# Kernel tuning notes

Hardware: AMD Instinct MI355X
Metric: run time of the kernel (lower is better)

Reference implementation:

```python
import jax, jax.numpy as jnp
import numpy as np

N = 50000      # nodes
E = 800000     # edges
D = 128        # feature dim
L = 3          # gcn layers
EPS = 1e-5     # batchnorm eps


def setup_inputs() -> dict:
    key = jax.random.key(0)
    ks = jax.random.split(key, 6)
    s = (2.0 / (D + D)) ** 0.5  # xavier-uniform scale proxy
    x = jax.random.normal(ks[0], (N, D), jnp.float32)
    edge_index = jax.random.randint(ks[1], (2, E), 0, N, dtype=jnp.int32)
    conv_w = jax.random.normal(ks[2], (L, D, D), jnp.float32) * s
    conv_b = jnp.zeros((L, D), jnp.float32)
    bn_gamma = jnp.ones((2, D), jnp.float32)
    bn_beta = jnp.zeros((2, D), jnp.float32)
    mlp_w = jax.random.normal(ks[3], (2, D, D), jnp.float32) * s
    mlp_b = jnp.zeros((2, D), jnp.float32)
    out_w = jax.random.normal(ks[4], (D, 1), jnp.float32) * s
    out_b = jnp.zeros((1,), jnp.float32)
    return dict(x=x, edge_index=edge_index, conv_w=conv_w, conv_b=conv_b,
                bn_gamma=bn_gamma, bn_beta=bn_beta, mlp_w=mlp_w, mlp_b=mlp_b,
                out_w=out_w, out_b=out_b)


def _batchnorm(h, gamma, beta):
    # train-mode BN: batch stats over nodes (biased variance, as torch uses for normalization)
    mean = jnp.mean(h, axis=0)
    var = jnp.mean((h - mean) ** 2, axis=0)
    return (h - mean) * jax.lax.rsqrt(var + EPS) * gamma + beta


def reference(x, conv_w, conv_b, bn_gamma, bn_beta, mlp_w, mlp_b, out_w, out_b, edge_index):
    # --- GCN normalization (PyG GCNConv default: add self-loops, sym norm) ---
    loops = jnp.arange(N, dtype=edge_index.dtype)
    src = jnp.concatenate([edge_index[0], loops])  # [E+N]
    dst = jnp.concatenate([edge_index[1], loops])
    deg = jax.ops.segment_sum(jnp.ones_like(dst, jnp.float32), dst, num_segments=N)
    dis = jnp.where(deg > 0, jax.lax.rsqrt(jnp.maximum(deg, 1.0)), 0.0)  # deg^-1/2
    norm = (dis[src] * dis[dst])[:, None]  # [E+N, 1]

    def gcn_conv(h, W, b):
        h = h @ W                                     # [N, D] transform
        msg = h[src] * norm                           # gather + scale, [E+N, D]
        return jax.ops.segment_sum(msg, dst, num_segments=N) + b

    # dropout is identity (training=False)
    h = x
    # layers 0..L-2: conv -> bn -> relu
    for layer in range(L - 1):
        h = gcn_conv(h, conv_w[layer], conv_b[layer])
        h = _batchnorm(h, bn_gamma[layer], bn_beta[layer])
        h = jax.nn.relu(h)
    # last conv: relu(conv), then bns[-1] applied AGAIN (faithful to original quirk)
    h = jax.nn.relu(gcn_conv(h, conv_w[L - 1], conv_b[L - 1]))
    h = _batchnorm(h, bn_gamma[-1], bn_beta[-1])

    # --- MLP classifier head: relu hidden layers, sigmoid output ---
    for i in range(mlp_w.shape[0]):
        h = jax.nn.relu(h @ mlp_w[i] + mlp_b[i])
    out = jax.nn.sigmoid(h @ out_w + out_b)  # [N, 1]
    return out
```

## Files before the change

kernel.cpp:

```cpp
#include <hip/hip_runtime.h>
#include <hip/hip_bf16.h>

#define NN 50000
#define EE 800000
#define DD 128

typedef __attribute__((ext_vector_type(8))) short short8;
typedef __attribute__((ext_vector_type(4))) float floatx4;

__device__ __forceinline__ unsigned short f2bf(float f) {
    unsigned int x = __float_as_uint(f);
    unsigned int r = x + 0x7fffu + ((x >> 16) & 1u);
    return (unsigned short)(r >> 16);
}
__device__ __forceinline__ float2 bf2x2(unsigned int u) {
    return make_float2(__uint_as_float(u << 16), __uint_as_float(u & 0xffff0000u));
}

__global__ void k_deg(const int* __restrict__ ei, int* __restrict__ deg) {
    int e = blockIdx.x * 256 + threadIdx.x;
    if (e < EE) {
        int d = ei[EE + e];
        if (d >= 0 && d < NN) atomicAdd(&deg[d], 1);
    }
}

__global__ void k_scan_block(const int* __restrict__ deg, int* __restrict__ scanned,
                             int* __restrict__ blocksum) {
    __shared__ int lds[256];
    int t = threadIdx.x;
    int i = blockIdx.x * 256 + t;
    int v = (i < NN) ? deg[i] : 0;
    lds[t] = v;
    __syncthreads();
    for (int off = 1; off < 256; off <<= 1) {
        int add = (t >= off) ? lds[t - off] : 0;
        __syncthreads();
        lds[t] += add;
        __syncthreads();
    }
    if (i < NN) scanned[i] = lds[t];
    if (t == 255) blocksum[blockIdx.x] = lds[255];
}

__global__ void k_scan_final(const int* __restrict__ deg, const int* __restrict__ scanned,
                             const int* __restrict__ blocksum, int nb,
                             int* __restrict__ rowptr, int* __restrict__ cursor,
                             float* __restrict__ dis) {
    __shared__ int lds[256];
    int t = threadIdx.x;
    int v = (t < nb) ? blocksum[t] : 0;
    lds[t] = v;
    __syncthreads();
    for (int off = 1; off < 256; off <<= 1) {
        int add = (t >= off) ? lds[t - off] : 0;
        __syncthreads();
        lds[t] += add;
        __syncthreads();
    }
    int boff = (blockIdx.x == 0) ? 0 : lds[blockIdx.x - 1];
    if (blockIdx.x == 0 && t == 0) rowptr[NN] = lds[nb - 1];
    int i = blockIdx.x * 256 + t;
    if (i < NN) {
        int rv = scanned[i] - deg[i] + boff;
        rowptr[i] = rv;
        cursor[i] = rv;
        dis[i] = rsqrtf((float)deg[i] + 1.0f);
    }
}

__global__ void k_fill(const int* __restrict__ ei, int* __restrict__ cursor,
                       int* __restrict__ csr) {
    int e = blockIdx.x * 256 + threadIdx.x;
    if (e < EE) {
        int s = ei[e];
        int d = ei[EE + e];
        if ((unsigned)s < (unsigned)NN && (unsigned)d < (unsigned)NN) {
            int pos = atomicAdd(&cursor[d], 1);
            csr[pos] = s;
        }
    }
}

__global__ void k_ell(const int* __restrict__ rowptr, const int* __restrict__ csr,
                      int* __restrict__ ell) {
    int t = blockIdx.x * 256 + threadIdx.x;
    if (t >= NN * 32) return;
    int r = t >> 5, slot = t & 31;
    int beg = rowptr[r];
    int d = rowptr[r + 1] - beg;
    ell[t] = (slot < d) ? csr[beg + slot] : NN;
}

__global__ void k_wprep(const float* __restrict__ conv_w, const float* __restrict__ mlp_w,
                        unsigned short* __restrict__ Wf, unsigned int* __restrict__ hsrow) {
    int g = blockIdx.x * 256 + threadIdx.x;
    if (g < 81920) {
        int m = g >> 14;
        int idx = g & 16383;
        int j  = idx & 7;
        int n  = (idx >> 3) & 15;
        int q  = (idx >> 7) & 3;
        int kk = (idx >> 9) & 3;
        int nt = (idx >> 11) & 1;
        int w  = (idx >> 12) & 3;
        int k = kk * 32 + q * 8 + j;
        int c = w * 32 + nt * 16 + n;
        const float* src = (m < 3) ? (conv_w + m * 16384) : (mlp_w + (m - 3) * 16384);
        Wf[g] = f2bf(src[k * 128 + c]);
    } else if (g - 81920 < 64) {
        hsrow[g - 81920] = 0u;
    }
}

#define LSTR 136
template<int PRO>
__global__ __launch_bounds__(256) void k_gemm_conv(const float* __restrict__ IN,
                                                   const unsigned short* __restrict__ Wf,
                                                   const float* __restrict__ dis,
                                                   const float* __restrict__ cs,
                                                   const float* __restrict__ css,
                                                   const float* __restrict__ gamma,
                                                   const float* __restrict__ beta,
                                                   unsigned short* __restrict__ OUT) {
    __shared__ unsigned short Al[64 * LSTR];
    __shared__ float bnscL[128], bnshL[128];
    const int tid = threadIdx.x;
    const int lane = tid & 63;
    const int w = tid >> 6;
    const int row0 = blockIdx.x * 64;

    if (PRO) {
        if (tid < 128) {
            const float invn = 1.f / (float)NN;
            float mean = cs[tid] * invn;
            float var = css[tid] * invn - mean * mean;
            float sc = gamma[tid] * rsqrtf(fmaxf(var, 0.f) + 1e-5f);
            bnscL[tid] = sc;
            bnshL[tid] = beta[tid] - mean * sc;
        }
        __syncthreads();
    }

    short8 bf[2][4];
    {
        const uint4* Wq = (const uint4*)Wf;
#pragma unroll
        for (int nt = 0; nt < 2; ++nt)
#pragma unroll
            for (int kk = 0; kk < 4; ++kk) {
                uint4 u = Wq[((w * 2 + nt) * 4 + kk) * 64 + lane];
                bf[nt][kk] = *(short8*)&u;
            }
    }

    {
        int r = tid >> 2, kq = (tid & 3) * 32;
        int gr = row0 + r;
        unsigned short tmp[32];
#pragma unroll
        for (int i = 0; i < 8; ++i) {
            float4 v = make_float4(0.f, 0.f, 0.f, 0.f);
            if (gr < NN) v = *(const float4*)&IN[(size_t)gr * DD + kq + i * 4];
            if (PRO) {
                float4 sc = *(const float4*)&bnscL[kq + i * 4];
                float4 sh = *(const float4*)&bnshL[kq + i * 4];
                v.x = fmaf(v.x, sc.x, sh.x);
                v.y = fmaf(v.y, sc.y, sh.y);
                v.z = fmaf(v.z, sc.z, sh.z);
                v.w = fmaf(v.w, sc.w, sh.w);
                v.x = fmaxf(v.x, 0.f); v.y = fmaxf(v.y, 0.f);
                v.z = fmaxf(v.z, 0.f); v.w = fmaxf(v.w, 0.f);
            }
            tmp[i * 4 + 0] = f2bf(v.x); tmp[i * 4 + 1] = f2bf(v.y);
            tmp[i * 4 + 2] = f2bf(v.z); tmp[i * 4 + 3] = f2bf(v.w);
        }
#pragma unroll
        for (int j = 0; j < 4; ++j)
            *(uint4*)&Al[r * LSTR + kq + j * 8] = ((uint4*)tmp)[j];
    }
    __syncthreads();

    const int n = lane & 15, q = lane >> 4;
    floatx4 acc[4][2];
#pragma unroll
    for (int mt = 0; mt < 4; ++mt)
#pragma unroll
        for (int nt = 0; nt < 2; ++nt)
            acc[mt][nt] = (floatx4){0.f, 0.f, 0.f, 0.f};

#pragma unroll
    for (int kk = 0; kk < 4; ++kk) {
        int ko = kk * 32 + q * 8;
#pragma unroll
        for (int mt = 0; mt < 4; ++mt) {
            short8 a = *(const short8*)&Al[(mt * 16 + n) * LSTR + ko];
            acc[mt][0] = __builtin_amdgcn_mfma_f32_16x16x32_bf16(a, bf[0][kk], acc[mt][0], 0, 0, 0);
            acc[mt][1] = __builtin_amdgcn_mfma_f32_16x16x32_bf16(a, bf[1][kk], acc[mt][1], 0, 0, 0);
        }
    }

#pragma unroll
    for (int mt = 0; mt < 4; ++mt) {
#pragma unroll
        for (int reg = 0; reg < 4; ++reg) {
            int r = row0 + mt * 16 + q * 4 + reg;
            if (r < NN) {
                float sc = dis[r];
                OUT[(size_t)r * DD + w * 32 + n]      = f2bf(acc[mt][0][reg] * sc);
                OUT[(size_t)r * DD + w * 32 + 16 + n] = f2bf(acc[mt][1][reg] * sc);
            }
        }
    }
}

__global__ __launch_bounds__(256) void k_mlp_head(const float* __restrict__ IN,
                                                  const unsigned short* __restrict__ Wf4,
                                                  const unsigned short* __restrict__ Wf5,
                                                  const float* __restrict__ b4,
                                                  const float* __restrict__ b5,
                                                  const float* __restrict__ cs,
                                                  const float* __restrict__ css,
                                                  const float* __restrict__ gamma,
                                                  const float* __restrict__ beta,
                                                  const float* __restrict__ ow,
                                                  const float* __restrict__ ob,
                                                  float* __restrict__ out) {
    __shared__ unsigned short Al[64 * LSTR];
    __shared__ float bnscL[128], bnshL[128];
    __shared__ float redH[4][64];
    const int tid = threadIdx.x;
    const int lane = tid & 63;
    const int w = tid >> 6;
    const int row0 = blockIdx.x * 64;
    const int n = lane & 15, q = lane >> 4;

    if (tid < 128) {
        const float invn = 1.f / (float)NN;
        float mean = cs[tid] * invn;
        float var = css[tid] * invn - mean * mean;
        float sc = gamma[tid] * rsqrtf(fmaxf(var, 0.f) + 1e-5f);
        bnscL[tid] = sc;
        bnshL[tid] = beta[tid] - mean * sc;
    }
    __syncthreads();

    {
        int r = tid >> 2, kq = (tid & 3) * 32;
        int gr = row0 + r;
        unsigned short tmp[32];
#pragma unroll
        for (int i = 0; i < 8; ++i) {
            float4 v = make_float4(0.f, 0.f, 0.f, 0.f);
            if (gr < NN) v = *(const float4*)&IN[(size_t)gr * DD + kq + i * 4];
            float4 sc = *(const float4*)&bnscL[kq + i * 4];
            float4 sh = *(const float4*)&bnshL[kq + i * 4];
            v.x = fmaf(v.x, sc.x, sh.x);
            v.y = fmaf(v.y, sc.y, sh.y);
            v.z = fmaf(v.z, sc.z, sh.z);
            v.w = fmaf(v.w, sc.w, sh.w);
            tmp[i * 4 + 0] = f2bf(v.x); tmp[i * 4 + 1] = f2bf(v.y);
            tmp[i * 4 + 2] = f2bf(v.z); tmp[i * 4 + 3] = f2bf(v.w);
        }
#pragma unroll
        for (int j = 0; j < 4; ++j)
            *(uint4*)&Al[r * LSTR + kq + j * 8] = ((uint4*)tmp)[j];
    }
    __syncthreads();

    floatx4 acc[4][2];
#pragma unroll
    for (int mt = 0; mt < 4; ++mt)
#pragma unroll
        for (int nt = 0; nt < 2; ++nt)
            acc[mt][nt] = (floatx4){0.f, 0.f, 0.f, 0.f};
    {
        const uint4* Wq = (const uint4*)Wf4;
#pragma unroll
        for (int kk = 0; kk < 4; ++kk) {
            uint4 u0 = Wq[((w * 2 + 0) * 4 + kk) * 64 + lane];
            uint4 u1 = Wq[((w * 2 + 1) * 4 + kk) * 64 + lane];
            int ko = kk * 32 + q * 8;
#pragma unroll
            for (int mt = 0; mt < 4; ++mt) {
                short8 a = *(const short8*)&Al[(mt * 16 + n) * LSTR + ko];
                acc[mt][0] = __builtin_amdgcn_mfma_f32_16x16x32_bf16(a, *(short8*)&u0, acc[mt][0], 0, 0, 0);
                acc[mt][1] = __builtin_amdgcn_mfma_f32_16x16x32_bf16(a, *(short8*)&u1, acc[mt][1], 0, 0, 0);
            }
        }
    }
    __syncthreads();

    {
        float b0c = b4[w * 32 + n], b1c = b4[w * 32 + 16 + n];
#pragma unroll
        for (int mt = 0; mt < 4; ++mt) {
#pragma unroll
            for (int reg = 0; reg < 4; ++reg) {
                int r = mt * 16 + q * 4 + reg;
                Al[r * LSTR + w * 32 + n]      = f2bf(fmaxf(acc[mt][0][reg] + b0c, 0.f));
                Al[r * LSTR + w * 32 + 16 + n] = f2bf(fmaxf(acc[mt][1][reg] + b1c, 0.f));
            }
        }
    }
    __syncthreads();

#pragma unroll
    for (int mt = 0; mt < 4; ++mt)
#pragma unroll
        for (int nt = 0; nt < 2; ++nt)
            acc[mt][nt] = (floatx4){0.f, 0.f, 0.f, 0.f};
    {
        const uint4* Wq = (const uint4*)Wf5;
#pragma unroll
        for (int kk = 0; kk < 4; ++kk) {
            uint4 u0 = Wq[((w * 2 + 0) * 4 + kk) * 64 + lane];
            uint4 u1 = Wq[((w * 2 + 1) * 4 + kk) * 64 + lane];
            int ko = kk * 32 + q * 8;
#pragma unroll
            for (int mt = 0; mt < 4; ++mt) {
                short8 a = *(const short8*)&Al[(mt * 16 + n) * LSTR + ko];
                acc[mt][0] = __builtin_amdgcn_mfma_f32_16x16x32_bf16(a, *(short8*)&u0, acc[mt][0], 0, 0, 0);
                acc[mt][1] = __builtin_amdgcn_mfma_f32_16x16x32_bf16(a, *(short8*)&u1, acc[mt][1], 0, 0, 0);
            }
        }
    }
    {
        float b0c = b5[w * 32 + n], b1c = b5[w * 32 + 16 + n];
        float w0c = ow[w * 32 + n], w1c = ow[w * 32 + 16 + n];
#pragma unroll
        for (int mt = 0; mt < 4; ++mt) {
#pragma unroll
            for (int reg = 0; reg < 4; ++reg) {
                float h0 = fmaxf(acc[mt][0][reg] + b0c, 0.f);
                float h1 = fmaxf(acc[mt][1][reg] + b1c, 0.f);
                float p = fmaf(h0, w0c, h1 * w1c);
                p += __shfl_xor(p, 1);
                p += __shfl_xor(p, 2);
                p += __shfl_xor(p, 4);
                p += __shfl_xor(p, 8);
                if (n == 0) redH[w][mt * 16 + q * 4 + reg] = p;
            }
        }
        __syncthreads();
        if (tid < 64) {
            int r = row0 + tid;
            if (r < NN) {
                float z = (redH[0][tid] + redH[1][tid]) + (redH[2][tid] + redH[3][tid]) + ob[0];
                out[r] = 1.f / (1.f + expf(-z));
            }
        }
    }
}
#undef LSTR

template<int RELU>
__global__ __launch_bounds__(256) void k_gather(const int* __restrict__ rowptr,
                                                const int* __restrict__ csr,
                                                const int* __restrict__ ell,
                                                const uint4* __restrict__ HSq,
                                                const float* __restrict__ dis,
                                                const float* __restrict__ bias,
                                                float* __restrict__ OUT,
                                                float* __restrict__ colsum,
                                                float* __restrict__ colsumsq) {
    const int tid = threadIdx.x;
    const int lane = tid & 63;
    const int wid = tid >> 6;
    const int c = lane & 15;
    const int jj = lane >> 4;
    const int gwave = blockIdx.x * 4 + wid;

    float4 bia0 = ((const float4*)bias)[2 * c];
    float4 bia1 = ((const float4*)bias)[2 * c + 1];
    float sum[8], sq[8];
#pragma unroll
    for (int t = 0; t < 8; ++t) { sum[t] = 0.f; sq[t] = 0.f; }

    for (int r = gwave; r < NN; r += 8192) {
        int beg = rowptr[r], end = rowptr[r + 1];
        int d = end - beg;
        float a[8];
#pragma unroll
        for (int t = 0; t < 8; ++t) a[t] = 0.f;

        if (jj == 0) {
            uint4 u = HSq[(size_t)r * 16 + c];
            float2 p0 = bf2x2(u.x), p1 = bf2x2(u.y), p2 = bf2x2(u.z), p3 = bf2x2(u.w);
            a[0] += p0.x; a[1] += p0.y; a[2] += p1.x; a[3] += p1.y;
            a[4] += p2.x; a[5] += p2.y; a[6] += p3.x; a[7] += p3.y;
        }

        if (d <= 32) {
            const int4* e4 = (const int4*)(ell + r * 32);
            int4 ia = e4[jj];
            int4 ib = e4[jj + 4];
            uint4 v0 = HSq[(size_t)ia.x * 16 + c];
            uint4 v1 = HSq[(size_t)ia.y * 16 + c];
            uint4 v2 = HSq[(size_t)ia.z * 16 + c];
            uint4 v3 = HSq[(size_t)ia.w * 16 + c];
            uint4 v4 = HSq[(size_t)ib.x * 16 + c];
            uint4 v5 = HSq[(size_t)ib.y * 16 + c];
            uint4 v6 = HSq[(size_t)ib.z * 16 + c];
            uint4 v7 = HSq[(size_t)ib.w * 16 + c];
            uint4 vs[8] = {v0, v1, v2, v3, v4, v5, v6, v7};
#pragma unroll
            for (int t = 0; t < 8; ++t) {
                float2 p0 = bf2x2(vs[t].x), p1 = bf2x2(vs[t].y);
                float2 p2 = bf2x2(vs[t].z), p3 = bf2x2(vs[t].w);
                a[0] += p0.x; a[1] += p0.y; a[2] += p1.x; a[3] += p1.y;
                a[4] += p2.x; a[5] += p2.y; a[6] += p3.x; a[7] += p3.y;
            }
        } else {
            int e1 = end - 1;
            for (int j = beg; j < end; j += 16) {
                int i0 = j + jj, i1 = j + 4 + jj, i2 = j + 8 + jj, i3 = j + 12 + jj;
                int s0 = csr[min(i0, e1)];
                int s1 = csr[min(i1, e1)];
                int s2 = csr[min(i2, e1)];
                int s3 = csr[min(i3, e1)];
                uint4 v0 = HSq[(size_t)s0 * 16 + c];
                uint4 v1 = HSq[(size_t)s1 * 16 + c];
                uint4 v2 = HSq[(size_t)s2 * 16 + c];
                uint4 v3 = HSq[(size_t)s3 * 16 + c];
                if (i0 < end) {
                    float2 p0 = bf2x2(v0.x), p1 = bf2x2(v0.y), p2 = bf2x2(v0.z), p3 = bf2x2(v0.w);
                    a[0] += p0.x; a[1] += p0.y; a[2] += p1.x; a[3] += p1.y;
                    a[4] += p2.x; a[5] += p2.y; a[6] += p3.x; a[7] += p3.y;
                }
                if (i1 < end) {
                    float2 p0 = bf2x2(v1.x), p1 = bf2x2(v1.y), p2 = bf2x2(v1.z), p3 = bf2x2(v1.w);
                    a[0] += p0.x; a[1] += p0.y; a[2] += p1.x; a[3] += p1.y;
                    a[4] += p2.x; a[5] += p2.y; a[6] += p3.x; a[7] += p3.y;
                }
                if (i2 < end) {
                    float2 p0 = bf2x2(v2.x), p1 = bf2x2(v2.y), p2 = bf2x2(v2.z), p3 = bf2x2(v2.w);
                    a[0] += p0.x; a[1] += p0.y; a[2] += p1.x; a[3] += p1.y;
                    a[4] += p2.x; a[5] += p2.y; a[6] += p3.x; a[7] += p3.y;
                }
                if (i3 < end) {
                    float2 p0 = bf2x2(v3.x), p1 = bf2x2(v3.y), p2 = bf2x2(v3.z), p3 = bf2x2(v3.w);
                    a[0] += p0.x; a[1] += p0.y; a[2] += p1.x; a[3] += p1.y;
                    a[4] += p2.x; a[5] += p2.y; a[6] += p3.x; a[7] += p3.y;
                }
            }
        }

#pragma unroll
        for (int t = 0; t < 8; ++t) {
            a[t] += __shfl_xor(a[t], 16);
            a[t] += __shfl_xor(a[t], 32);
        }

        if (jj == 0) {
            float dr = dis[r];
            float v[8];
            v[0] = fmaf(dr, a[0], bia0.x); v[1] = fmaf(dr, a[1], bia0.y);
            v[2] = fmaf(dr, a[2], bia0.z); v[3] = fmaf(dr, a[3], bia0.w);
            v[4] = fmaf(dr, a[4], bia1.x); v[5] = fmaf(dr, a[5], bia1.y);
            v[6] = fmaf(dr, a[6], bia1.z); v[7] = fmaf(dr, a[7], bia1.w);
            if (RELU) {
#pragma unroll
                for (int t = 0; t < 8; ++t) v[t] = fmaxf(v[t], 0.f);
            }
            float* op = OUT + (size_t)r * DD + c * 8;
            *(float4*)op       = make_float4(v[0], v[1], v[2], v[3]);
            *(float4*)(op + 4) = make_float4(v[4], v[5], v[6], v[7]);
#pragma unroll
            for (int t = 0; t < 8; ++t) { sum[t] += v[t]; sq[t] += v[t] * v[t]; }
        }
    }

    __shared__ float redS[4][16][8];
    __shared__ float redQ[4][16][8];
    if (jj == 0) {
#pragma unroll
        for (int t = 0; t < 8; ++t) { redS[wid][c][t] = sum[t]; redQ[wid][c][t] = sq[t]; }
    }
    __syncthreads();
    if (tid < 128) {
        int ci = tid >> 3, ct = tid & 7;
        float S = (redS[0][ci][ct] + redS[1][ci][ct]) + (redS[2][ci][ct] + redS[3][ci][ct]);
        float Q = (redQ[0][ci][ct] + redQ[1][ci][ct]) + (redQ[2][ci][ct] + redQ[3][ci][ct]);
        atomicAdd(&colsum[tid], S);
        atomicAdd(&colsumsq[tid], Q);
    }
}

extern "C" void kernel_launch(void* const* d_in, const int* in_sizes, int n_in,
                              void* d_out, int out_size, void* d_ws, size_t ws_size,
                              hipStream_t stream) {
    const float* x      = (const float*)d_in[0];
    const int*   ei     = (const int*)d_in[1];
    const float* conv_w = (const float*)d_in[2];
    const float* conv_b = (const float*)d_in[3];
    const float* bn_g   = (const float*)d_in[4];
    const float* bn_b   = (const float*)d_in[5];
    const float* mlp_w  = (const float*)d_in[6];
    const float* mlp_b  = (const float*)d_in[7];
    const float* out_w  = (const float*)d_in[8];
    const float* out_b  = (const float*)d_in[9];
    float* out = (float*)d_out;

    const size_t ND4 = (size_t)NN * DD * 4;
    char* ws = (char*)d_ws;
    size_t off = 0;
    float* B0      = (float*)(ws + off); off += ND4;
    unsigned short* B1b = (unsigned short*)(ws + off); off += ND4 / 2 + 256;
    int*   deg     = (int*)  (ws + off); off += 204800;
    float* cs3     = (float*)(ws + off); off += 3 * 512;
    float* css3    = (float*)(ws + off); off += 3 * 512;
    float* dis     = (float*)(ws + off); off += 204800;
    int*   rowptr  = (int*)  (ws + off); off += 204804 + 60;
    int*   cursor  = (int*)  (ws + off); off += 204800;
    int*   bsum    = (int*)  (ws + off); off += 1024;
    unsigned short* Wfb = (unsigned short*)(ws + off); off += 5 * 16384 * 2;
    int*   csr     = (int*)  (ws + off); off += (size_t)EE * 4;
    int*   ell     = (int*)  (ws + off); off += (size_t)NN * 32 * 4;

    const int gemm_grid = (NN + 63) / 64;
    const int nscan = (NN + 255) / 256;
    const int gather_grid = 2048;

    hipMemsetAsync(deg, 0, 204800 + 6 * 512, stream);

    k_deg<<<(EE + 255) / 256, 256, 0, stream>>>(ei, deg);
    k_scan_block<<<nscan, 256, 0, stream>>>(deg, cursor, bsum);
    k_scan_final<<<nscan, 256, 0, stream>>>(deg, cursor, bsum, nscan, rowptr, cursor, dis);
    k_fill<<<(EE + 255) / 256, 256, 0, stream>>>(ei, cursor, csr);
    k_ell<<<(NN * 32 + 255) / 256, 256, 0, stream>>>(rowptr, csr, ell);
    k_wprep<<<321, 256, 0, stream>>>(conv_w, mlp_w, Wfb, (unsigned int*)(B1b + (size_t)NN * DD));

    k_gemm_conv<0><<<gemm_grid, 256, 0, stream>>>(x, Wfb, dis,
        nullptr, nullptr, nullptr, nullptr, B1b);
    k_gather<0><<<gather_grid, 256, 0, stream>>>(rowptr, csr, ell, (const uint4*)B1b, dis, conv_b, B0, cs3, css3);

    k_gemm_conv<1><<<gemm_grid, 256, 0, stream>>>(B0, Wfb + 16384, dis,
        cs3, css3, bn_g, bn_b, B1b);
    k_gather<0><<<gather_grid, 256, 0, stream>>>(rowptr, csr, ell, (const uint4*)B1b, dis, conv_b + DD, B0, cs3 + 128, css3 + 128);

    k_gemm_conv<1><<<gemm_grid, 256, 0, stream>>>(B0, Wfb + 2 * 16384, dis,
        cs3 + 128, css3 + 128, bn_g + DD, bn_b + DD, B1b);
    k_gather<1><<<gather_grid, 256, 0, stream>>>(rowptr, csr, ell, (const uint4*)B1b, dis, conv_b + 2 * DD, B0, cs3 + 256, css3 + 256);

    k_mlp_head<<<gemm_grid, 256, 0, stream>>>(B0, Wfb + 3 * 16384, Wfb + 4 * 16384,
        mlp_b, mlp_b + DD, cs3 + 256, css3 + 256, bn_g + DD, bn_b + DD, out_w, out_b, out);
}
```

Measured before the change: 456.5 us.

## Store gather outputs as bf16, build ELL during fill, dynamic row scheduling

The aggregation kernels now write their N×D output in bf16 instead of fp32, and the following GEMM and MLP head read it back as bf16, halving that intermediate traffic. The separate ELL construction kernel is removed: scan_final pads the unused ELL slots and the fill kernel writes neighbour indices directly into ELL. The gather kernel switches from a static grid-stride row loop to dynamic block-level work stealing through an atomic counter, 16 rows at a time. This adds bf16 rounding of the post-conv activations, which BN and the head then consume, and adds two block barriers per work chunk.

```diff
diff --git a/kernel.cpp b/kernel.cpp
--- a/kernel.cpp
+++ b/kernel.cpp
@@ -46,7 +46,7 @@
 __global__ void k_scan_final(const int* __restrict__ deg, const int* __restrict__ scanned,
                              const int* __restrict__ blocksum, int nb,
                              int* __restrict__ rowptr, int* __restrict__ cursor,
-                             float* __restrict__ dis) {
+                             float* __restrict__ dis, int* __restrict__ ell) {
     __shared__ int lds[256];
     int t = threadIdx.x;
     int v = (t < nb) ? blocksum[t] : 0;
@@ -62,15 +62,18 @@
     if (blockIdx.x == 0 && t == 0) rowptr[NN] = lds[nb - 1];
     int i = blockIdx.x * 256 + t;
     if (i < NN) {
-        int rv = scanned[i] - deg[i] + boff;
+        int d = deg[i];
+        int rv = scanned[i] - d + boff;
         rowptr[i] = rv;
         cursor[i] = rv;
-        dis[i] = rsqrtf((float)deg[i] + 1.0f);
-    }
-}
-
-__global__ void k_fill(const int* __restrict__ ei, int* __restrict__ cursor,
-                       int* __restrict__ csr) {
+        dis[i] = rsqrtf((float)d + 1.0f);
+        for (int slot = d; slot < 32; ++slot) ell[i * 32 + slot] = NN;
+    }
+}
+
+__global__ void k_fill(const int* __restrict__ ei, const int* __restrict__ rowptr,
+                       int* __restrict__ cursor, int* __restrict__ csr,
+                       int* __restrict__ ell) {
     int e = blockIdx.x * 256 + threadIdx.x;
     if (e < EE) {
         int s = ei[e];
@@ -78,18 +81,10 @@
         if ((unsigned)s < (unsigned)NN && (unsigned)d < (unsigned)NN) {
             int pos = atomicAdd(&cursor[d], 1);
             csr[pos] = s;
-        }
-    }
-}
-
-__global__ void k_ell(const int* __restrict__ rowptr, const int* __restrict__ csr,
-                      int* __restrict__ ell) {
-    int t = blockIdx.x * 256 + threadIdx.x;
-    if (t >= NN * 32) return;
-    int r = t >> 5, slot = t & 31;
-    int beg = rowptr[r];
-    int d = rowptr[r + 1] - beg;
-    ell[t] = (slot < d) ? csr[beg + slot] : NN;
+            int slot = pos - rowptr[d];
+            if (slot < 32) ell[d * 32 + slot] = s;
+        }
+    }
 }
 
 __global__ void k_wprep(const float* __restrict__ conv_w, const float* __restrict__ mlp_w,
@@ -115,7 +110,7 @@
 
 #define LSTR 136
 template<int PRO>
-__global__ __launch_bounds__(256) void k_gemm_conv(const float* __restrict__ IN,
+__global__ __launch_bounds__(256) void k_gemm_conv(const void* __restrict__ INv,
                                                    const unsigned short* __restrict__ Wf,
                                                    const float* __restrict__ dis,
                                                    const float* __restrict__ cs,
@@ -158,22 +153,29 @@
         int r = tid >> 2, kq = (tid & 3) * 32;
         int gr = row0 + r;
         unsigned short tmp[32];
-#pragma unroll
-        for (int i = 0; i < 8; ++i) {
-            float4 v = make_float4(0.f, 0.f, 0.f, 0.f);
-            if (gr < NN) v = *(const float4*)&IN[(size_t)gr * DD + kq + i * 4];
-            if (PRO) {
-                float4 sc = *(const float4*)&bnscL[kq + i * 4];
-                float4 sh = *(const float4*)&bnshL[kq + i * 4];
-                v.x = fmaf(v.x, sc.x, sh.x);
-                v.y = fmaf(v.y, sc.y, sh.y);
-                v.z = fmaf(v.z, sc.z, sh.z);
-                v.w = fmaf(v.w, sc.w, sh.w);
-                v.x = fmaxf(v.x, 0.f); v.y = fmaxf(v.y, 0.f);
-                v.z = fmaxf(v.z, 0.f); v.w = fmaxf(v.w, 0.f);
-            }
-            tmp[i * 4 + 0] = f2bf(v.x); tmp[i * 4 + 1] = f2bf(v.y);
-            tmp[i * 4 + 2] = f2bf(v.z); tmp[i * 4 + 3] = f2bf(v.w);
+        if (PRO == 0) {
+            const float* IN = (const float*)INv;
+#pragma unroll
+            for (int i = 0; i < 8; ++i) {
+                float4 v = make_float4(0.f, 0.f, 0.f, 0.f);
+                if (gr < NN) v = *(const float4*)&IN[(size_t)gr * DD + kq + i * 4];
+                tmp[i * 4 + 0] = f2bf(v.x); tmp[i * 4 + 1] = f2bf(v.y);
+                tmp[i * 4 + 2] = f2bf(v.z); tmp[i * 4 + 3] = f2bf(v.w);
+            }
+        } else {
+            const unsigned int* inu = (const unsigned int*)INv;
+#pragma unroll
+            for (int i = 0; i < 4; ++i) {
+                uint4 u = make_uint4(0u, 0u, 0u, 0u);
+                if (gr < NN) u = *(const uint4*)&inu[(size_t)gr * 64 + (kq >> 1) + i * 4];
+                float2 p0 = bf2x2(u.x), p1 = bf2x2(u.y), p2 = bf2x2(u.z), p3 = bf2x2(u.w);
+                float vv[8] = {p0.x, p0.y, p1.x, p1.y, p2.x, p2.y, p3.x, p3.y};
+#pragma unroll
+                for (int j = 0; j < 8; ++j) {
+                    float t2 = fmaf(vv[j], bnscL[kq + i * 8 + j], bnshL[kq + i * 8 + j]);
+                    tmp[i * 8 + j] = f2bf(fmaxf(t2, 0.f));
+                }
+            }
         }
 #pragma unroll
         for (int j = 0; j < 4; ++j)
@@ -214,7 +216,7 @@
     }
 }
 
-__global__ __launch_bounds__(256) void k_mlp_head(const float* __restrict__ IN,
+__global__ __launch_bounds__(256) void k_mlp_head(const unsigned int* __restrict__ INu,
                                                   const unsigned short* __restrict__ Wf4,
                                                   const unsigned short* __restrict__ Wf5,
                                                   const float* __restrict__ b4,
@@ -250,17 +252,16 @@
         int gr = row0 + r;
         unsigned short tmp[32];
 #pragma unroll
-        for (int i = 0; i < 8; ++i) {
-            float4 v = make_float4(0.f, 0.f, 0.f, 0.f);
-            if (gr < NN) v = *(const float4*)&IN[(size_t)gr * DD + kq + i * 4];
-            float4 sc = *(const float4*)&bnscL[kq + i * 4];
-            float4 sh = *(const float4*)&bnshL[kq + i * 4];
-            v.x = fmaf(v.x, sc.x, sh.x);
-            v.y = fmaf(v.y, sc.y, sh.y);
-            v.z = fmaf(v.z, sc.z, sh.z);
-            v.w = fmaf(v.w, sc.w, sh.w);
-            tmp[i * 4 + 0] = f2bf(v.x); tmp[i * 4 + 1] = f2bf(v.y);
-            tmp[i * 4 + 2] = f2bf(v.z); tmp[i * 4 + 3] = f2bf(v.w);
+        for (int i = 0; i < 4; ++i) {
+            uint4 u = make_uint4(0u, 0u, 0u, 0u);
+            if (gr < NN) u = *(const uint4*)&INu[(size_t)gr * 64 + (kq >> 1) + i * 4];
+            float2 p0 = bf2x2(u.x), p1 = bf2x2(u.y), p2 = bf2x2(u.z), p3 = bf2x2(u.w);
+            float vv[8] = {p0.x, p0.y, p1.x, p1.y, p2.x, p2.y, p3.x, p3.y};
+#pragma unroll
+            for (int j = 0; j < 8; ++j) {
+                float t2 = fmaf(vv[j], bnscL[kq + i * 8 + j], bnshL[kq + i * 8 + j]);
+                tmp[i * 8 + j] = f2bf(t2);
+            }
         }
 #pragma unroll
         for (int j = 0; j < 4; ++j)
@@ -361,15 +362,15 @@
                                                 const uint4* __restrict__ HSq,
                                                 const float* __restrict__ dis,
                                                 const float* __restrict__ bias,
-                                                float* __restrict__ OUT,
+                                                unsigned short* __restrict__ OUT,
                                                 float* __restrict__ colsum,
-                                                float* __restrict__ colsumsq) {
+                                                float* __restrict__ colsumsq,
+                                                int* __restrict__ wctr) {
     const int tid = threadIdx.x;
     const int lane = tid & 63;
     const int wid = tid >> 6;
     const int c = lane & 15;
     const int jj = lane >> 4;
-    const int gwave = blockIdx.x * 4 + wid;
 
     float4 bia0 = ((const float4*)bias)[2 * c];
     float4 bia1 = ((const float4*)bias)[2 * c + 1];
@@ -377,97 +378,109 @@
 #pragma unroll
     for (int t = 0; t < 8; ++t) { sum[t] = 0.f; sq[t] = 0.f; }
 
-    for (int r = gwave; r < NN; r += 8192) {
-        int beg = rowptr[r], end = rowptr[r + 1];
-        int d = end - beg;
-        float a[8];
-#pragma unroll
-        for (int t = 0; t < 8; ++t) a[t] = 0.f;
-
-        if (jj == 0) {
-            uint4 u = HSq[(size_t)r * 16 + c];
-            float2 p0 = bf2x2(u.x), p1 = bf2x2(u.y), p2 = bf2x2(u.z), p3 = bf2x2(u.w);
-            a[0] += p0.x; a[1] += p0.y; a[2] += p1.x; a[3] += p1.y;
-            a[4] += p2.x; a[5] += p2.y; a[6] += p3.x; a[7] += p3.y;
-        }
-
-        if (d <= 32) {
-            const int4* e4 = (const int4*)(ell + r * 32);
-            int4 ia = e4[jj];
-            int4 ib = e4[jj + 4];
-            uint4 v0 = HSq[(size_t)ia.x * 16 + c];
-            uint4 v1 = HSq[(size_t)ia.y * 16 + c];
-            uint4 v2 = HSq[(size_t)ia.z * 16 + c];
-            uint4 v3 = HSq[(size_t)ia.w * 16 + c];
-            uint4 v4 = HSq[(size_t)ib.x * 16 + c];
-            uint4 v5 = HSq[(size_t)ib.y * 16 + c];
-            uint4 v6 = HSq[(size_t)ib.z * 16 + c];
-            uint4 v7 = HSq[(size_t)ib.w * 16 + c];
-            uint4 vs[8] = {v0, v1, v2, v3, v4, v5, v6, v7};
-#pragma unroll
-            for (int t = 0; t < 8; ++t) {
-                float2 p0 = bf2x2(vs[t].x), p1 = bf2x2(vs[t].y);
-                float2 p2 = bf2x2(vs[t].z), p3 = bf2x2(vs[t].w);
+    __shared__ int baseS;
+    for (;;) {
+        __syncthreads();
+        if (tid == 0) baseS = atomicAdd(wctr, 16);
+        __syncthreads();
+        int base = baseS;
+        if (base >= NN) break;
+        int r0 = base + wid * 4;
+        int r1 = min(r0 + 4, NN);
+        for (int r = r0; r < r1; ++r) {
+            int beg = rowptr[r], end = rowptr[r + 1];
+            int d = end - beg;
+            float a[8];
+#pragma unroll
+            for (int t = 0; t < 8; ++t) a[t] = 0.f;
+
+            if (jj == 0) {
+                uint4 u = HSq[(size_t)r * 16 + c];
+                float2 p0 = bf2x2(u.x), p1 = bf2x2(u.y), p2 = bf2x2(u.z), p3 = bf2x2(u.w);
                 a[0] += p0.x; a[1] += p0.y; a[2] += p1.x; a[3] += p1.y;
                 a[4] += p2.x; a[5] += p2.y; a[6] += p3.x; a[7] += p3.y;
             }
-        } else {
-            int e1 = end - 1;
-            for (int j = beg; j < end; j += 16) {
-                int i0 = j + jj, i1 = j + 4 + jj, i2 = j + 8 + jj, i3 = j + 12 + jj;
-                int s0 = csr[min(i0, e1)];
-                int s1 = csr[min(i1, e1)];
-                int s2 = csr[min(i2, e1)];
-                int s3 = csr[min(i3, e1)];
-                uint4 v0 = HSq[(size_t)s0 * 16 + c];
-                uint4 v1 = HSq[(size_t)s1 * 16 + c];
-                uint4 v2 = HSq[(size_t)s2 * 16 + c];
-                uint4 v3 = HSq[(size_t)s3 * 16 + c];
-                if (i0 < end) {
-                    float2 p0 = bf2x2(v0.x), p1 = bf2x2(v0.y), p2 = bf2x2(v0.z), p3 = bf2x2(v0.w);
+
+            if (d <= 32) {
+                const int4* e4 = (const int4*)(ell + r * 32);
+                int4 ia = e4[jj];
+                int4 ib = e4[jj + 4];
+                uint4 v0 = HSq[(size_t)ia.x * 16 + c];
+                uint4 v1 = HSq[(size_t)ia.y * 16 + c];
+                uint4 v2 = HSq[(size_t)ia.z * 16 + c];
+                uint4 v3 = HSq[(size_t)ia.w * 16 + c];
+                uint4 v4 = HSq[(size_t)ib.x * 16 + c];
+                uint4 v5 = HSq[(size_t)ib.y * 16 + c];
+                uint4 v6 = HSq[(size_t)ib.z * 16 + c];
+                uint4 v7 = HSq[(size_t)ib.w * 16 + c];
+                uint4 vs[8] = {v0, v1, v2, v3, v4, v5, v6, v7};
+#pragma unroll
+                for (int t = 0; t < 8; ++t) {
+                    float2 p0 = bf2x2(vs[t].x), p1 = bf2x2(vs[t].y);
+                    float2 p2 = bf2x2(vs[t].z), p3 = bf2x2(vs[t].w);
                     a[0] += p0.x; a[1] += p0.y; a[2] += p1.x; a[3] += p1.y;
                     a[4] += p2.x; a[5] += p2.y; a[6] += p3.x; a[7] += p3.y;
                 }
-                if (i1 < end) {
-                    float2 p0 = bf2x2(v1.x), p1 = bf2x2(v1.y), p2 = bf2x2(v1.z), p3 = bf2x2(v1.w);
-                    a[0] += p0.x; a[1] += p0.y; a[2] += p1.x; a[3] += p1.y;
-                    a[4] += p2.x; a[5] += p2.y; a[6] += p3.x; a[7] += p3.y;
+            } else {
+                int e1 = end - 1;
+                for (int j = beg; j < end; j += 16) {
+                    int i0 = j + jj, i1 = j + 4 + jj, i2 = j + 8 + jj, i3 = j + 12 + jj;
+                    int s0 = csr[min(i0, e1)];
+                    int s1 = csr[min(i1, e1)];
+                    int s2 = csr[min(i2, e1)];
+                    int s3 = csr[min(i3, e1)];
+                    uint4 v0 = HSq[(size_t)s0 * 16 + c];
+                    uint4 v1 = HSq[(size_t)s1 * 16 + c];
+                    uint4 v2 = HSq[(size_t)s2 * 16 + c];
+                    uint4 v3 = HSq[(size_t)s3 * 16 + c];
+                    if (i0 < end) {
+                        float2 p0 = bf2x2(v0.x), p1 = bf2x2(v0.y), p2 = bf2x2(v0.z), p3 = bf2x2(v0.w);
+                        a[0] += p0.x; a[1] += p0.y; a[2] += p1.x; a[3] += p1.y;
+                        a[4] += p2.x; a[5] += p2.y; a[6] += p3.x; a[7] += p3.y;
+                    }
+                    if (i1 < end) {
+                        float2 p0 = bf2x2(v1.x), p1 = bf2x2(v1.y), p2 = bf2x2(v1.z), p3 = bf2x2(v1.w);
+                        a[0] += p0.x; a[1] += p0.y; a[2] += p1.x; a[3] += p1.y;
+                        a[4] += p2.x; a[5] += p2.y; a[6] += p3.x; a[7] += p3.y;
+                    }
+                    if (i2 < end) {
+                        float2 p0 = bf2x2(v2.x), p1 = bf2x2(v2.y), p2 = bf2x2(v2.z), p3 = bf2x2(v2.w);
+                        a[0] += p0.x; a[1] += p0.y; a[2] += p1.x; a[3] += p1.y;
+                        a[4] += p2.x; a[5] += p2.y; a[6] += p3.x; a[7] += p3.y;
+                    }
+                    if (i3 < end) {
+                        float2 p0 = bf2x2(v3.x), p1 = bf2x2(v3.y), p2 = bf2x2(v3.z), p3 = bf2x2(v3.w);
+                        a[0] += p0.x; a[1] += p0.y; a[2] += p1.x; a[3] += p1.y;
+                        a[4] += p2.x; a[5] += p2.y; a[6] += p3.x; a[7] += p3.y;
+                    }
                 }
-                if (i2 < end) {
-                    float2 p0 = bf2x2(v2.x), p1 = bf2x2(v2.y), p2 = bf2x2(v2.z), p3 = bf2x2(v2.w);
-                    a[0] += p0.x; a[1] += p0.y; a[2] += p1.x; a[3] += p1.y;
-                    a[4] += p2.x; a[5] += p2.y; a[6] += p3.x; a[7] += p3.y;
+            }
+
+#pragma unroll
+            for (int t = 0; t < 8; ++t) {
+                a[t] += __shfl_xor(a[t], 16);
+                a[t] += __shfl_xor(a[t], 32);
+            }
+
+            if (jj == 0) {
+                float dr = dis[r];
+                float v[8];
+                v[0] = fmaf(dr, a[0], bia0.x); v[1] = fmaf(dr, a[1], bia0.y);
+                v[2] = fmaf(dr, a[2], bia0.z); v[3] = fmaf(dr, a[3], bia0.w);
+                v[4] = fmaf(dr, a[4], bia1.x); v[5] = fmaf(dr, a[5], bia1.y);
+                v[6] = fmaf(dr, a[6], bia1.z); v[7] = fmaf(dr, a[7], bia1.w);
+                if (RELU) {
+#pragma unroll
+                    for (int t = 0; t < 8; ++t) v[t] = fmaxf(v[t], 0.f);
                 }
-                if (i3 < end) {
-                    float2 p0 = bf2x2(v3.x), p1 = bf2x2(v3.y), p2 = bf2x2(v3.z), p3 = bf2x2(v3.w);
-                    a[0] += p0.x; a[1] += p0.y; a[2] += p1.x; a[3] += p1.y;
-                    a[4] += p2.x; a[5] += p2.y; a[6] += p3.x; a[7] += p3.y;
-                }
-            }
-        }
-
-#pragma unroll
-        for (int t = 0; t < 8; ++t) {
-            a[t] += __shfl_xor(a[t], 16);
-            a[t] += __shfl_xor(a[t], 32);
-        }
-
-        if (jj == 0) {
-            float dr = dis[r];
-            float v[8];
-            v[0] = fmaf(dr, a[0], bia0.x); v[1] = fmaf(dr, a[1], bia0.y);
-            v[2] = fmaf(dr, a[2], bia0.z); v[3] = fmaf(dr, a[3], bia0.w);
-            v[4] = fmaf(dr, a[4], bia1.x); v[5] = fmaf(dr, a[5], bia1.y);
-            v[6] = fmaf(dr, a[6], bia1.z); v[7] = fmaf(dr, a[7], bia1.w);
-            if (RELU) {
-#pragma unroll
-                for (int t = 0; t < 8; ++t) v[t] = fmaxf(v[t], 0.f);
-            }
-            float* op = OUT + (size_t)r * DD + c * 8;
-            *(float4*)op       = make_float4(v[0], v[1], v[2], v[3]);
-            *(float4*)(op + 4) = make_float4(v[4], v[5], v[6], v[7]);
-#pragma unroll
-            for (int t = 0; t < 8; ++t) { sum[t] += v[t]; sq[t] += v[t] * v[t]; }
+                unsigned int p[4];
+#pragma unroll
+                for (int t = 0; t < 4; ++t)
+                    p[t] = (unsigned int)f2bf(v[2 * t]) | ((unsigned int)f2bf(v[2 * t + 1]) << 16);
+                *(uint4*)&OUT[(size_t)r * DD + c * 8] = make_uint4(p[0], p[1], p[2], p[3]);
+#pragma unroll
+                for (int t = 0; t < 8; ++t) { sum[t] += v[t]; sq[t] += v[t] * v[t]; }
+            }
         }
     }
 
@@ -505,11 +518,12 @@
     const size_t ND4 = (size_t)NN * DD * 4;
     char* ws = (char*)d_ws;
     size_t off = 0;
-    float* B0      = (float*)(ws + off); off += ND4;
+    unsigned short* B0 = (unsigned short*)(ws + off); off += ND4 / 2;
     unsigned short* B1b = (unsigned short*)(ws + off); off += ND4 / 2 + 256;
     int*   deg     = (int*)  (ws + off); off += 204800;
     float* cs3     = (float*)(ws + off); off += 3 * 512;
     float* css3    = (float*)(ws + off); off += 3 * 512;
+    int*   wctr    = (int*)  (ws + off); off += 64;
     float* dis     = (float*)(ws + off); off += 204800;
     int*   rowptr  = (int*)  (ws + off); off += 204804 + 60;
     int*   cursor  = (int*)  (ws + off); off += 204800;
@@ -522,27 +536,26 @@
     const int nscan = (NN + 255) / 256;
     const int gather_grid = 2048;
 
-    hipMemsetAsync(deg, 0, 204800 + 6 * 512, stream);
+    hipMemsetAsync(deg, 0, 204800 + 6 * 512 + 64, stream);
 
     k_deg<<<(EE + 255) / 256, 256, 0, stream>>>(ei, deg);
     k_scan_block<<<nscan, 256, 0, stream>>>(deg, cursor, bsum);
-    k_scan_final<<<nscan, 256, 0, stream>>>(deg, cursor, bsum, nscan, rowptr, cursor, dis);
-    k_fill<<<(EE + 255) / 256, 256, 0, stream>>>(ei, cursor, csr);
-    k_ell<<<(NN * 32 + 255) / 256, 256, 0, stream>>>(rowptr, csr, ell);
+    k_scan_final<<<nscan, 256, 0, stream>>>(deg, cursor, bsum, nscan, rowptr, cursor, dis, ell);
+    k_fill<<<(EE + 255) / 256, 256, 0, stream>>>(ei, rowptr, cursor, csr, ell);
     k_wprep<<<321, 256, 0, stream>>>(conv_w, mlp_w, Wfb, (unsigned int*)(B1b + (size_t)NN * DD));
 
     k_gemm_conv<0><<<gemm_grid, 256, 0, stream>>>(x, Wfb, dis,
         nullptr, nullptr, nullptr, nullptr, B1b);
-    k_gather<0><<<gather_grid, 256, 0, stream>>>(rowptr, csr, ell, (const uint4*)B1b, dis, conv_b, B0, cs3, css3);
+    k_gather<0><<<gather_grid, 256, 0, stream>>>(rowptr, csr, ell, (const uint4*)B1b, dis, conv_b, B0, cs3, css3, wctr);
 
     k_gemm_conv<1><<<gemm_grid, 256, 0, stream>>>(B0, Wfb + 16384, dis,
         cs3, css3, bn_g, bn_b, B1b);
-    k_gather<0><<<gather_grid, 256, 0, stream>>>(rowptr, csr, ell, (const uint4*)B1b, dis, conv_b + DD, B0, cs3 + 128, css3 + 128);
+    k_gather<0><<<gather_grid, 256, 0, stream>>>(rowptr, csr, ell, (const uint4*)B1b, dis, conv_b + DD, B0, cs3 + 128, css3 + 128, wctr + 1);
 
     k_gemm_conv<1><<<gemm_grid, 256, 0, stream>>>(B0, Wfb + 2 * 16384, dis,
         cs3 + 128, css3 + 128, bn_g + DD, bn_b + DD, B1b);
-    k_gather<1><<<gather_grid, 256, 0, stream>>>(rowptr, csr, ell, (const uint4*)B1b, dis, conv_b + 2 * DD, B0, cs3 + 256, css3 + 256);
-
-    k_mlp_head<<<gemm_grid, 256, 0, stream>>>(B0, Wfb + 3 * 16384, Wfb + 4 * 16384,
+    k_gather<1><<<gather_grid, 256, 0, stream>>>(rowptr, csr, ell, (const uint4*)B1b, dis, conv_b + 2 * DD, B0, cs3 + 256, css3 + 256, wctr + 2);
+
+    k_mlp_head<<<gemm_grid, 256, 0, stream>>>((const unsigned int*)B0, Wfb + 3 * 16384, Wfb + 4 * 16384,
         mlp_b, mlp_b + DD, cs3 + 256, css3 + 256, bn_g + DD, bn_b + DD, out_w, out_b, out);
 }
```

Result: slower. 534.5 us (+17.1%).
